# Performance work log

Measured on AMD Instinct MI355X. Metric: run time of the kernel, lower is better.

Reference implementation:

```python
import jax, jax.numpy as jnp
import numpy as np

SQRT_D = 32  # ceil(sqrt(d_out)) with d_out = 1024
D_OUT = 1024


def setup_inputs() -> dict:
    key = jax.random.key(0)
    k1, k2, k3 = jax.random.split(key, 3)
    x = jax.random.normal(k1, (8, 4096, 1024), dtype=jnp.float32)
    scale = 1.0 / np.sqrt(SQRT_D)
    L = jax.random.normal(k2, (SQRT_D, SQRT_D, SQRT_D), dtype=jnp.float32) * scale
    R = jax.random.normal(k3, (SQRT_D, SQRT_D, SQRT_D), dtype=jnp.float32) * scale
    return {"x": x, "L": L, "R": R}


def reference(x, L, R):
    # MonarchOutProjection with proj_type == 'Monarch' (d_in*n_heads == d_out,
    # hd == sqrt_d**2 so no padding). Monarch: permute -> blockdiag(L) ->
    # permute -> blockdiag(R) -> permute, then slice to d_out.
    b, n, hd = x.shape
    s = SQRT_D
    # rearrange '... (m n) -> ... (n m)': view (m, n) then transpose.
    h = x.reshape(b, n, s, s)          # (..., m, n_inner)
    h = jnp.swapaxes(h, -1, -2)        # (..., block, inner)
    # blockdiag_matmul with L: einsum 'bnm,...bm->...bn'
    h = jnp.einsum('bnm,...bm->...bn', L, h)
    # rearrange '... (m n) -> ... (n m)' on the flattened result == transpose
    h = jnp.swapaxes(h, -1, -2)
    # blockdiag_matmul with R
    h = jnp.einsum('bnm,...bm->...bn', R, h)
    # final rearrange '... (m n) -> ... (n m)'
    h = jnp.swapaxes(h, -1, -2)
    out = h.reshape(b, n, hd)
    return out[..., :D_OUT]
```

## Files before the change

### kernel.cpp

```cpp
#include <hip/hip_runtime.h>


typedef __attribute__((ext_vector_type(8))) short short8;
typedef __attribute__((ext_vector_type(4))) float floatx4;

__device__ __forceinline__ unsigned int f2bf(float f) {
    unsigned int u = __float_as_uint(f);
    return (u + 0x7fffu + ((u >> 16) & 1u)) >> 16;
}
__device__ __forceinline__ unsigned int pack2bf(float a, float b) {
    return f2bf(a) | (f2bf(b) << 16);
}
__device__ __forceinline__ float bf2f(unsigned int u16) {
    return __uint_as_float(u16 << 16);
}

__global__ __launch_bounds__(256, 2)
void monarch_kernel(const float* __restrict__ x,
                    const float* __restrict__ L,
                    const float* __restrict__ R,
                    float* __restrict__ out) {
    __shared__ __align__(16) unsigned short xs [16][1024];
    __shared__ __align__(16) unsigned short y1s[16][1024];

    const int tid  = threadIdx.x;
    const int w    = tid >> 6;
    const int lane = tid & 63;
    const int tl   = lane & 15;
    const int quad = lane >> 4;
    const long tok0 = (long)blockIdx.x * 16;

    {
        const int c = tid * 4;
        #pragma unroll
        for (int t = 0; t < 16; ++t) {
            const float4 v = *(const float4*)(x + (tok0 + t) * 1024 + c);
            *(unsigned int*)&xs[t][(c    ) ^ (2 * t)] = pack2bf(v.x, v.y);
            *(unsigned int*)&xs[t][(c + 2) ^ (2 * t)] = pack2bf(v.z, v.w);
        }
    }
    __syncthreads();

    {
        const int xsw = 2 * tl;
        #pragma unroll
        for (int pp = 0; pp < 8; ++pp) {
            const int p  = w * 8 + pp;
            const int pX = p ^ xsw;
            short8 b1;
            #pragma unroll
            for (int j = 0; j < 8; ++j)
                b1[j] = (short)xs[tl][quad * 256 + j * 32 + pX];
            #pragma unroll
            for (int qt = 0; qt < 2; ++qt) {
                const int q = qt * 16 + tl;
                const float* lp = L + ((p * 32 + q) * 32 + quad * 8);
                const float4 la = *(const float4*)lp;
                const float4 lb = *(const float4*)(lp + 4);
                short8 a1;
                a1[0] = (short)f2bf(la.x); a1[1] = (short)f2bf(la.y);
                a1[2] = (short)f2bf(la.z); a1[3] = (short)f2bf(la.w);
                a1[4] = (short)f2bf(lb.x); a1[5] = (short)f2bf(lb.y);
                a1[6] = (short)f2bf(lb.z); a1[7] = (short)f2bf(lb.w);
                floatx4 acc = {0.f, 0.f, 0.f, 0.f};
                acc = __builtin_amdgcn_mfma_f32_16x16x32_bf16(a1, b1, acc, 0, 0, 0);
                #pragma unroll
                for (int r = 0; r < 4; ++r) {
                    const int qo = qt * 16 + quad * 4 + r;
                    y1s[tl][(qo * 32 + p) ^ xsw] = (unsigned short)f2bf(acc[r]);
                }
            }
        }
    }
    __syncthreads();

    {
        const int xsw = 2 * tl;
        #pragma unroll
        for (int qq = 0; qq < 8; ++qq) {
            const int q = w * 8 + qq;
            short8 b2;
            #pragma unroll
            for (int j = 0; j < 8; ++j)
                b2[j] = (short)y1s[tl][(q * 32 + quad * 8 + j) ^ xsw];
            #pragma unroll
            for (int rt = 0; rt < 2; ++rt) {
                const int r = rt * 16 + tl;
                const float* rp = R + ((q * 32 + r) * 32 + quad * 8);
                const float4 ra = *(const float4*)rp;
                const float4 rb = *(const float4*)(rp + 4);
                short8 a2;
                a2[0] = (short)f2bf(ra.x); a2[1] = (short)f2bf(ra.y);
                a2[2] = (short)f2bf(ra.z); a2[3] = (short)f2bf(ra.w);
                a2[4] = (short)f2bf(rb.x); a2[5] = (short)f2bf(rb.y);
                a2[6] = (short)f2bf(rb.z); a2[7] = (short)f2bf(rb.w);
                floatx4 acc = {0.f, 0.f, 0.f, 0.f};
                acc = __builtin_amdgcn_mfma_f32_16x16x32_bf16(a2, b2, acc, 0, 0, 0);
                #pragma unroll
                for (int r4 = 0; r4 < 4; ++r4) {
                    const int ro = rt * 16 + quad * 4 + r4;
                    xs[tl][(ro * 32 + q) ^ xsw] = (unsigned short)f2bf(acc[r4]);
                }
            }
        }
    }
    __syncthreads();

    {
        const int c = tid * 4;
        #pragma unroll
        for (int t = 0; t < 16; ++t) {
            const unsigned int u0 = *(const unsigned int*)&xs[t][(c    ) ^ (2 * t)];
            const unsigned int u1 = *(const unsigned int*)&xs[t][(c + 2) ^ (2 * t)];
            float4 o;
            o.x = bf2f(u0 & 0xffffu); o.y = bf2f(u0 >> 16);
            o.z = bf2f(u1 & 0xffffu); o.w = bf2f(u1 >> 16);
            *(float4*)(out + (tok0 + t) * 1024 + c) = o;
        }
    }
}

extern "C" void kernel_launch(void* const* d_in, const int* in_sizes, int n_in,
                              void* d_out, int out_size, void* d_ws, size_t ws_size,
                              hipStream_t stream) {
    const float* x = (const float*)d_in[0];
    const float* L = (const float*)d_in[1];
    const float* R = (const float*)d_in[2];
    float* out = (float*)d_out;

    const int n_tokens = 8 * 4096;
    const int grid = n_tokens / 16;
    monarch_kernel<<<grid, 256, 0, stream>>>(x, L, R, out);
}
```

Before: 281.1 us.

## Pre-pack weights to bf16 MFMA layout, share one LDS buffer, raise occupancy

Adds a small prep kernel that converts L and R to bf16 once per call and stores them in the per-lane MFMA fragment order in workspace. The main kernel then loads each weight fragment with a single 16-byte load instead of doing fp32 loads and conversions in every block. The intermediate and output now reuse a single 16 KB LDS buffer, with the second-stage results held in registers until after a barrier. This halves shared memory per block so launch bounds can be raised to 4 blocks per SIMD. The cost is an extra kernel launch and higher register pressure from the 16 accumulators.

```diff
diff --git a/kernel.cpp b/kernel.cpp
--- a/kernel.cpp
+++ b/kernel.cpp
@@ -1,4 +1,5 @@
 #include <hip/hip_runtime.h>
+#include <hip/hip_bf16.h>
 
 
 typedef __attribute__((ext_vector_type(8))) short short8;
@@ -9,19 +10,40 @@
     return (u + 0x7fffu + ((u >> 16) & 1u)) >> 16;
 }
 __device__ __forceinline__ unsigned int pack2bf(float a, float b) {
-    return f2bf(a) | (f2bf(b) << 16);
+    __hip_bfloat162 h = __float22bfloat162_rn(float2{a, b});
+    return *(unsigned int*)&h;
 }
 __device__ __forceinline__ float bf2f(unsigned int u16) {
     return __uint_as_float(u16 << 16);
 }
 
-__global__ __launch_bounds__(256, 2)
+__global__ void prep_weights(const float* __restrict__ L, const float* __restrict__ R,
+                             unsigned short* __restrict__ Lb, unsigned short* __restrict__ Rb) {
+    const int t = blockIdx.x * 256 + threadIdx.x;
+    const float* src        = (t < 4096) ? L : R;
+    unsigned short* dst     = (t < 4096) ? Lb : Rb;
+    const int i    = t & 4095;
+    const int lane = i & 63;
+    const int pq   = i >> 6;
+    const int p    = pq >> 1;
+    const int qt   = pq & 1;
+    const int q    = qt * 16 + (lane & 15);
+    const int m0   = (lane >> 4) * 8;
+    const float* s = src + (p * 32 + q) * 32 + m0;
+    uint4 o;
+    o.x = pack2bf(s[0], s[1]);
+    o.y = pack2bf(s[2], s[3]);
+    o.z = pack2bf(s[4], s[5]);
+    o.w = pack2bf(s[6], s[7]);
+    *(uint4*)(dst + (size_t)i * 8) = o;
+}
+
+__global__ __launch_bounds__(256, 4)
 void monarch_kernel(const float* __restrict__ x,
-                    const float* __restrict__ L,
-                    const float* __restrict__ R,
+                    const unsigned short* __restrict__ Lb,
+                    const unsigned short* __restrict__ Rb,
                     float* __restrict__ out) {
-    __shared__ __align__(16) unsigned short xs [16][1024];
-    __shared__ __align__(16) unsigned short y1s[16][1024];
+    __shared__ __align__(16) unsigned short buf[16][1024];
 
     const int tid  = threadIdx.x;
     const int w    = tid >> 6;
@@ -35,8 +57,8 @@
         #pragma unroll
         for (int t = 0; t < 16; ++t) {
             const float4 v = *(const float4*)(x + (tok0 + t) * 1024 + c);
-            *(unsigned int*)&xs[t][(c    ) ^ (2 * t)] = pack2bf(v.x, v.y);
-            *(unsigned int*)&xs[t][(c + 2) ^ (2 * t)] = pack2bf(v.z, v.w);
+            *(unsigned int*)&buf[t][(c    ) ^ (2 * t)] = pack2bf(v.x, v.y);
+            *(unsigned int*)&buf[t][(c + 2) ^ (2 * t)] = pack2bf(v.z, v.w);
         }
     }
     __syncthreads();
@@ -50,25 +72,37 @@
             short8 b1;
             #pragma unroll
             for (int j = 0; j < 8; ++j)
-                b1[j] = (short)xs[tl][quad * 256 + j * 32 + pX];
+                b1[j] = (short)buf[tl][quad * 256 + j * 32 + pX];
             #pragma unroll
             for (int qt = 0; qt < 2; ++qt) {
-                const int q = qt * 16 + tl;
-                const float* lp = L + ((p * 32 + q) * 32 + quad * 8);
-                const float4 la = *(const float4*)lp;
-                const float4 lb = *(const float4*)(lp + 4);
-                short8 a1;
-                a1[0] = (short)f2bf(la.x); a1[1] = (short)f2bf(la.y);
-                a1[2] = (short)f2bf(la.z); a1[3] = (short)f2bf(la.w);
-                a1[4] = (short)f2bf(lb.x); a1[5] = (short)f2bf(lb.y);
-                a1[6] = (short)f2bf(lb.z); a1[7] = (short)f2bf(lb.w);
+                const short8 a1 = *(const short8*)(Lb + (size_t)((p * 2 + qt) * 64 + lane) * 8);
                 floatx4 acc = {0.f, 0.f, 0.f, 0.f};
                 acc = __builtin_amdgcn_mfma_f32_16x16x32_bf16(a1, b1, acc, 0, 0, 0);
                 #pragma unroll
                 for (int r = 0; r < 4; ++r) {
                     const int qo = qt * 16 + quad * 4 + r;
-                    y1s[tl][(qo * 32 + p) ^ xsw] = (unsigned short)f2bf(acc[r]);
+                    buf[tl][qo * 32 + pX] = (unsigned short)f2bf(acc[r]);
                 }
+            }
+        }
+    }
+    __syncthreads();
+
+    floatx4 acc2[8][2];
+    {
+        const int xsw = 2 * tl;
+        #pragma unroll
+        for (int qq = 0; qq < 8; ++qq) {
+            const int q = w * 8 + qq;
+            short8 b2;
+            #pragma unroll
+            for (int j = 0; j < 8; ++j)
+                b2[j] = (short)buf[tl][q * 32 + ((quad * 8 + j) ^ xsw)];
+            #pragma unroll
+            for (int rt = 0; rt < 2; ++rt) {
+                const short8 a2 = *(const short8*)(Rb + (size_t)((q * 2 + rt) * 64 + lane) * 8);
+                floatx4 z = {0.f, 0.f, 0.f, 0.f};
+                acc2[qq][rt] = __builtin_amdgcn_mfma_f32_16x16x32_bf16(a2, b2, z, 0, 0, 0);
             }
         }
     }
@@ -78,28 +112,14 @@
         const int xsw = 2 * tl;
         #pragma unroll
         for (int qq = 0; qq < 8; ++qq) {
-            const int q = w * 8 + qq;
-            short8 b2;
-            #pragma unroll
-            for (int j = 0; j < 8; ++j)
-                b2[j] = (short)y1s[tl][(q * 32 + quad * 8 + j) ^ xsw];
+            const int q  = w * 8 + qq;
+            const int qX = q ^ xsw;
             #pragma unroll
             for (int rt = 0; rt < 2; ++rt) {
-                const int r = rt * 16 + tl;
-                const float* rp = R + ((q * 32 + r) * 32 + quad * 8);
-                const float4 ra = *(const float4*)rp;
-                const float4 rb = *(const float4*)(rp + 4);
-                short8 a2;
-                a2[0] = (short)f2bf(ra.x); a2[1] = (short)f2bf(ra.y);
-                a2[2] = (short)f2bf(ra.z); a2[3] = (short)f2bf(ra.w);
-                a2[4] = (short)f2bf(rb.x); a2[5] = (short)f2bf(rb.y);
-                a2[6] = (short)f2bf(rb.z); a2[7] = (short)f2bf(rb.w);
-                floatx4 acc = {0.f, 0.f, 0.f, 0.f};
-                acc = __builtin_amdgcn_mfma_f32_16x16x32_bf16(a2, b2, acc, 0, 0, 0);
                 #pragma unroll
                 for (int r4 = 0; r4 < 4; ++r4) {
                     const int ro = rt * 16 + quad * 4 + r4;
-                    xs[tl][(ro * 32 + q) ^ xsw] = (unsigned short)f2bf(acc[r4]);
+                    buf[tl][ro * 32 + qX] = (unsigned short)f2bf(acc2[qq][rt][r4]);
                 }
             }
         }
@@ -110,8 +130,8 @@
         const int c = tid * 4;
         #pragma unroll
         for (int t = 0; t < 16; ++t) {
-            const unsigned int u0 = *(const unsigned int*)&xs[t][(c    ) ^ (2 * t)];
-            const unsigned int u1 = *(const unsigned int*)&xs[t][(c + 2) ^ (2 * t)];
+            const unsigned int u0 = *(const unsigned int*)&buf[t][(c    ) ^ (2 * t)];
+            const unsigned int u1 = *(const unsigned int*)&buf[t][(c + 2) ^ (2 * t)];
             float4 o;
             o.x = bf2f(u0 & 0xffffu); o.y = bf2f(u0 >> 16);
             o.z = bf2f(u1 & 0xffffu); o.w = bf2f(u1 >> 16);
@@ -128,7 +148,12 @@
     const float* R = (const float*)d_in[2];
     float* out = (float*)d_out;
 
+    unsigned short* Lb = (unsigned short*)d_ws;
+    unsigned short* Rb = Lb + 32768;
+
+    prep_weights<<<32, 256, 0, stream>>>(L, R, Lb, Rb);
+
     const int n_tokens = 8 * 4096;
     const int grid = n_tokens / 16;
-    monarch_kernel<<<grid, 256, 0, stream>>>(x, L, R, out);
+    monarch_kernel<<<grid, 256, 0, stream>>>(x, Lb, Rb, out);
 }
```

Result: faster. 242.1 us (-13.9%).
